# Kernel optimization log

Measured on AMD Instinct MI355X. Metric: run time of the kernel, lower is better.

The kernel has to match this reference:

```python
import jax, jax.numpy as jnp
import numpy as np

NUM_ITEMS = 50000
EMB = 16
SLATE = 10
HID = 512
LAT = 64
RESP = 1024
BATCH = 256


def _linear_params(k, out_dim, in_dim):
    kw, kb = jax.random.split(k)
    s = 1.0 / np.sqrt(in_dim)
    W = jax.random.uniform(kw, (out_dim, in_dim), jnp.float32, -s, s)
    b = jax.random.uniform(kb, (out_dim,), jnp.float32, -s, s)
    return W, b


def setup_inputs() -> dict:
    key = jax.random.key(0)
    ks = jax.random.split(key, 10)
    user_repr = jax.random.randint(ks[0], (BATCH, NUM_ITEMS), 0, 2, dtype=jnp.int32)
    slate = jax.random.randint(ks[1], (BATCH, SLATE), 0, NUM_ITEMS, dtype=jnp.int32)
    response_encoded = jax.random.uniform(ks[2], (BATCH, RESP), jnp.float32)
    eps = jax.random.normal(ks[3], (BATCH, LAT), jnp.float32)
    emb = jax.random.normal(ks[4], (NUM_ITEMS, EMB), jnp.float32)
    in_enc = SLATE * EMB + EMB + RESP
    W_enc, b_enc = _linear_params(ks[5], HID, in_enc)
    W_mu, b_mu = _linear_params(ks[6], LAT, HID)
    W_lv, b_lv = _linear_params(ks[7], LAT, HID)
    in_dec = LAT + EMB + RESP
    W_d1, b_d1 = _linear_params(ks[8], HID, in_dec)
    W_d2, b_d2 = _linear_params(ks[9], SLATE * EMB, HID)
    return {"user_repr": user_repr, "slate": slate, "response_encoded": response_encoded,
            "eps": eps, "emb": emb, "W_enc": W_enc, "b_enc": b_enc,
            "W_mu": W_mu, "b_mu": b_mu, "W_lv": W_lv, "b_lv": b_lv,
            "W_d1": W_d1, "b_d1": b_d1, "W_d2": W_d2, "b_d2": b_d2}


def reference(user_repr, slate, response_encoded, eps, emb,
              W_enc, b_enc, W_mu, b_mu, W_lv, b_lv, W_d1, b_d1, W_d2, b_d2):
    # Ragged embedding-mean pooling over interacted items (vectorized segment mean):
    # mean of emb rows where user_repr==1  ==  (indicator @ emb) / count
    uf = user_repr.astype(jnp.float32)                       # [B, N]
    counts = jnp.sum(uf, axis=1, keepdims=True)              # [B, 1]
    user = (uf @ emb) / counts                               # [B, E]

    cond = jnp.concatenate([user, response_encoded], axis=1)  # [B, E+R]
    slate_emb = emb[slate]                                    # [B, K, E]
    slate_vec = slate_emb.reshape(-1, SLATE * EMB)            # [B, K*E]
    x = jnp.concatenate([slate_vec, cond], axis=1)

    # encoder
    h = jax.nn.relu(x @ W_enc.T + b_enc)
    z_mean = h @ W_mu.T + b_mu
    z_log_var = h @ W_lv.T + b_lv

    # reparameterized sample
    z = z_mean + eps * jnp.exp(0.5 * z_log_var)

    # decoder
    dz = jnp.concatenate([z, cond], axis=1)
    dh = jax.nn.relu(dz @ W_d1.T + b_d1)
    rx = jax.nn.relu(dh @ W_d2.T + b_d2)                      # [B, K*E]
    rx = rx.reshape(-1, SLATE, EMB)                           # [B, K, E]

    # scores vs all items, softmax over items
    logits = jnp.einsum('bkh,nh->bkn', rx, emb)               # [B, K, N]
    probs = jax.nn.softmax(logits, axis=2)
    recon_slate = jnp.argmax(probs, axis=2)                   # [B, K]
    recon_resp = jnp.take_along_axis(probs, slate[:, :, None], axis=2)[..., 0]  # [B, K]
    return z_mean, z_log_var, recon_slate, recon_resp
```

## Files before the change

### kernel.cpp

```cpp
#include <hip/hip_runtime.h>

#define NITEMS 50000
#define EMBD   16
#define NSLATE 10
#define HIDD   512
#define LATD   64
#define RESPD  1024
#define BATCH  256
#define PCHUNK 3125
#define LOG2E  1.44269504088896340736f
#define SHIFT  64.0f

#define NCOL   2560
#define NT     1563
#define IC     64
#define TPC    25

#define OUT_ZM 0
#define OUT_ZLV 16384
#define OUT_RS 32768
#define OUT_RR 35328

#define WS_X    0
#define WS_DZ   307200
#define WS_P2   0
#define WS_PP   589824
#define WS_PART 589824
#define WS_PS   589824
#define WS_PM   753664
#define WS_PA   917504
#define WS_RX   1114112
#define WS_RXS0 1155072
#define WS_RXS1 1175552
#define WS_RXS2 1196032

typedef __attribute__((ext_vector_type(8))) short bfrag;
typedef __attribute__((ext_vector_type(16))) float f32x16;

__device__ __forceinline__ float bfround(float v) {
  unsigned u = __float_as_uint(v);
  unsigned r = (u + 0x7FFFu + ((u >> 16) & 1u)) & 0xFFFF0000u;
  return __uint_as_float(r);
}
__device__ __forceinline__ float bftrunc(float v) {
  return __uint_as_float(__float_as_uint(v) & 0xFFFF0000u);
}
__device__ __forceinline__ short bf16bits(float v) {
  return (short)(__float_as_uint(v) >> 16);
}

__global__ __launch_bounds__(256) void pool_part(const int* __restrict__ u,
    const float* __restrict__ emb, float* __restrict__ pp) {
  int b = blockIdx.x, c = blockIdx.y, t = threadIdx.x;
  float acc[16];
  #pragma unroll
  for (int i = 0; i < 16; ++i) acc[i] = 0.0f;
  float cnt = 0.0f;
  const int* ub = u + (size_t)b * NITEMS;
  int n1 = c * PCHUNK + PCHUNK;
  for (int n = c * PCHUNK + t; n < n1; n += 256) {
    if (ub[n]) {
      const float4* e4 = (const float4*)(emb + (size_t)n * 16);
      float4 a = e4[0], bb = e4[1], cc = e4[2], dd = e4[3];
      acc[0] += a.x;  acc[1] += a.y;  acc[2] += a.z;  acc[3] += a.w;
      acc[4] += bb.x; acc[5] += bb.y; acc[6] += bb.z; acc[7] += bb.w;
      acc[8] += cc.x; acc[9] += cc.y; acc[10] += cc.z; acc[11] += cc.w;
      acc[12] += dd.x; acc[13] += dd.y; acc[14] += dd.z; acc[15] += dd.w;
      cnt += 1.0f;
    }
  }
  #pragma unroll
  for (int off = 32; off > 0; off >>= 1) {
    #pragma unroll
    for (int i = 0; i < 16; ++i) acc[i] += __shfl_down(acc[i], off);
    cnt += __shfl_down(cnt, off);
  }
  int lane = t & 63, wv = t >> 6;
  if (lane == 0) {
    float* dst = pp + ((size_t)(b * 16 + c) * 4 + wv) * 17;
    #pragma unroll
    for (int i = 0; i < 16; ++i) dst[i] = acc[i];
    dst[16] = cnt;
  }
}

__global__ __launch_bounds__(256) void build_x(const float* __restrict__ pp,
    const int* __restrict__ slate, const float* __restrict__ resp,
    const float* __restrict__ emb, float* __restrict__ x, float* __restrict__ dz) {
  __shared__ float fin[17];
  int b = blockIdx.x, t = threadIdx.x;
  if (t < 17) {
    float a = 0.f;
    const float* p = pp + (size_t)b * 64 * 17 + t;
    #pragma unroll
    for (int w = 0; w < 64; ++w) a += p[w * 17];
    fin[t] = a;
  }
  __syncthreads();
  float inv = 1.0f / fin[16];
  if (t < 16) {
    float uv = fin[t] * inv;
    x[b * 1200 + 160 + t] = uv;
    dz[b * 1104 + 64 + t] = uv;
  }
  if (t >= 32 && t < 192) {
    int i = t - 32;
    int k = i >> 4, e = i & 15;
    int it = slate[b * 10 + k];
    x[b * 1200 + i] = emb[(size_t)it * 16 + e];
  }
  for (int i = t; i < 1024; i += 256) {
    float r = resp[b * 1024 + i];
    x[b * 1200 + 176 + i] = r;
    dz[b * 1104 + 80 + i] = r;
  }
}

__global__ __launch_bounds__(256) void gemm64(const float* __restrict__ A,
    const float* __restrict__ B, float* __restrict__ P, int M, int N, int K, int kChunk) {
  __shared__ float As[16][68];
  __shared__ float Bs[16][68];
  int tid = threadIdx.x;
  int m0 = blockIdx.y * 64, n0 = blockIdx.x * 64;
  int ks = blockIdx.z * kChunk;
  int ke = ks + kChunk; if (ke > K) ke = K;
  int sr = tid >> 2;
  int sc = (tid & 3) * 4;
  int tx = tid & 15, ty = tid >> 4;
  float acc[4][4];
  #pragma unroll
  for (int i = 0; i < 4; ++i)
    #pragma unroll
    for (int j = 0; j < 4; ++j) acc[i][j] = 0.f;
  for (int k0 = ks; k0 < ke; k0 += 16) {
    float4 av = make_float4(0.f, 0.f, 0.f, 0.f);
    float4 bv = make_float4(0.f, 0.f, 0.f, 0.f);
    if (k0 + sc < ke)
      av = *(const float4*)(A + (size_t)(m0 + sr) * K + k0 + sc);
    if (k0 + sc < ke && n0 + sr < N)
      bv = *(const float4*)(B + (size_t)(n0 + sr) * K + k0 + sc);
    __syncthreads();
    As[sc][sr] = av.x; As[sc + 1][sr] = av.y; As[sc + 2][sr] = av.z; As[sc + 3][sr] = av.w;
    Bs[sc][sr] = bv.x; Bs[sc + 1][sr] = bv.y; Bs[sc + 2][sr] = bv.z; Bs[sc + 3][sr] = bv.w;
    __syncthreads();
    #pragma unroll
    for (int kk = 0; kk < 16; ++kk) {
      float4 a4 = *(const float4*)&As[kk][4 * ty];
      float4 b4 = *(const float4*)&Bs[kk][4 * tx];
      float a[4] = {a4.x, a4.y, a4.z, a4.w};
      float b[4] = {b4.x, b4.y, b4.z, b4.w};
      #pragma unroll
      for (int i = 0; i < 4; ++i)
        #pragma unroll
        for (int j = 0; j < 4; ++j) acc[i][j] = fmaf(a[i], b[j], acc[i][j]);
    }
  }
  float* Pz = P + (size_t)blockIdx.z * M * N;
  #pragma unroll
  for (int i = 0; i < 4; ++i) {
    int m = m0 + 4 * ty + i, n = n0 + 4 * tx;
    if (n < N)
      *(float4*)(Pz + (size_t)m * N + n) = make_float4(acc[i][0], acc[i][1], acc[i][2], acc[i][3]);
  }
}

__global__ __launch_bounds__(128) void mulv_z_kernel(const float* __restrict__ part,
    const float* __restrict__ benc,
    const float* __restrict__ Wmu, const float* __restrict__ bmu,
    const float* __restrict__ Wlv, const float* __restrict__ blv,
    const float* __restrict__ eps, float* __restrict__ out, float* __restrict__ dz) {
  __shared__ __align__(16) float hs[512];
  __shared__ float zms[64], zlvs[64];
  int b = blockIdx.x, t = threadIdx.x;
  for (int i = t; i < 512; i += 128) {
    float a = benc[i];
    #pragma unroll
    for (int s = 0; s < 4; ++s) a += part[(size_t)s * 131072 + b * 512 + i];
    hs[i] = fmaxf(a, 0.f);
  }
  __syncthreads();
  const float* Wr = (t < 64) ? (Wmu + (size_t)t * 512) : (Wlv + (size_t)(t - 64) * 512);
  float bias = (t < 64) ? bmu[t] : blv[t - 64];
  const float4* w4 = (const float4*)Wr;
  const float4* h4 = (const float4*)hs;
  float a0 = 0.f, a1 = 0.f, a2 = 0.f, a3 = 0.f;
  #pragma unroll 4
  for (int i = 0; i < 128; ++i) {
    float4 w = w4[i], hv = h4[i];
    a0 = fmaf(w.x, hv.x, a0); a1 = fmaf(w.y, hv.y, a1);
    a2 = fmaf(w.z, hv.z, a2); a3 = fmaf(w.w, hv.w, a3);
  }
  float acc = (a0 + a1) + (a2 + a3) + bias;
  if (t < 64) { out[OUT_ZM + b * 64 + t] = acc; zms[t] = acc; }
  else        { out[OUT_ZLV + b * 64 + (t - 64)] = acc; zlvs[t - 64] = acc; }
  __syncthreads();
  if (t < 64) {
    float zv = fmaf(eps[b * 64 + t], __builtin_amdgcn_exp2f(0.7213475204444817f * zlvs[t]), zms[t]);
    dz[b * 1104 + t] = zv;
  }
}

__global__ __launch_bounds__(256) void gemm_d2(const float* __restrict__ part,
    const float* __restrict__ bd1, const float* __restrict__ W, float* __restrict__ p2) {
  __shared__ float As[16][68];
  __shared__ float Bs[16][68];
  const int N = 160;
  int tid = threadIdx.x;
  int m0 = blockIdx.y * 64, n0 = blockIdx.x * 64;
  int ks = blockIdx.z * 64, ke = ks + 64;
  int sr = tid >> 2, sc = (tid & 3) * 4;
  int tx = tid & 15, ty = tid >> 4;
  float acc[4][4];
  #pragma unroll
  for (int i = 0; i < 4; ++i)
    #pragma unroll
    for (int j = 0; j < 4; ++j) acc[i][j] = 0.f;
  for (int k0 = ks; k0 < ke; k0 += 16) {
    int col = k0 + sc;
    const float* p = part + (size_t)(m0 + sr) * 512 + col;
    float4 a0 = *(const float4*)(p);
    float4 a1 = *(const float4*)(p + 131072);
    float4 a2 = *(const float4*)(p + 262144);
    float4 a3 = *(const float4*)(p + 393216);
    float4 bb = *(const float4*)(bd1 + col);
    float4 av;
    av.x = fmaxf(a0.x + a1.x + a2.x + a3.x + bb.x, 0.f);
    av.y = fmaxf(a0.y + a1.y + a2.y + a3.y + bb.y, 0.f);
    av.z = fmaxf(a0.z + a1.z + a2.z + a3.z + bb.z, 0.f);
    av.w = fmaxf(a0.w + a1.w + a2.w + a3.w + bb.w, 0.f);
    float4 bv = make_float4(0.f, 0.f, 0.f, 0.f);
    if (n0 + sr < N)
      bv = *(const float4*)(W + (size_t)(n0 + sr) * 512 + col);
    __syncthreads();
    As[sc][sr] = av.x; As[sc + 1][sr] = av.y; As[sc + 2][sr] = av.z; As[sc + 3][sr] = av.w;
    Bs[sc][sr] = bv.x; Bs[sc + 1][sr] = bv.y; Bs[sc + 2][sr] = bv.z; Bs[sc + 3][sr] = bv.w;
    __syncthreads();
    #pragma unroll
    for (int kk = 0; kk < 16; ++kk) {
      float4 a4 = *(const float4*)&As[kk][4 * ty];
      float4 b4 = *(const float4*)&Bs[kk][4 * tx];
      float a[4] = {a4.x, a4.y, a4.z, a4.w};
      float b[4] = {b4.x, b4.y, b4.z, b4.w};
      #pragma unroll
      for (int i = 0; i < 4; ++i)
        #pragma unroll
        for (int j = 0; j < 4; ++j) acc[i][j] = fmaf(a[i], b[j], acc[i][j]);
    }
  }
  float* Pz = p2 + (size_t)blockIdx.z * 40960;
  #pragma unroll
  for (int i = 0; i < 4; ++i) {
    int m = m0 + 4 * ty + i, n = n0 + 4 * tx;
    if (n < N)
      *(float4*)(Pz + (size_t)m * 160 + n) = make_float4(acc[i][0], acc[i][1], acc[i][2], acc[i][3]);
  }
}

__global__ __launch_bounds__(256) void rx_prep(const float* __restrict__ p2,
    const float* __restrict__ bd2, float* __restrict__ rx,
    unsigned short* __restrict__ rx0, unsigned short* __restrict__ rx1,
    unsigned short* __restrict__ rx2) {
  int b = blockIdx.x, t = threadIdx.x;
  if (t >= 160) return;
  float a = bd2[t];
  #pragma unroll
  for (int z = 0; z < 8; ++z) a += p2[(size_t)z * 40960 + b * 160 + t];
  float v = fmaxf(a, 0.f) * LOG2E;
  rx[b * 160 + t] = v;
  int col = b * 10 + (t >> 4), e = t & 15;
  float f0 = bfround(v);
  float d1 = v - f0;
  float f1 = bfround(d1);
  float d2 = d1 - f1;
  float f2 = bfround(d2);
  rx0[col * 16 + e] = (unsigned short)(__float_as_uint(f0) >> 16);
  rx1[col * 16 + e] = (unsigned short)(__float_as_uint(f1) >> 16);
  rx2[col * 16 + e] = (unsigned short)(__float_as_uint(f2) >> 16);
}

__global__ __launch_bounds__(256) void score_mfma(const float* __restrict__ emb,
    const unsigned short* __restrict__ rx0, const unsigned short* __restrict__ rx1,
    const unsigned short* __restrict__ rx2,
    float* __restrict__ ps, float* __restrict__ pm, int* __restrict__ pa) {
  int t = threadIdx.x;
  int w = t >> 6, l = t & 63;
  int ln = l & 31, hf = l >> 5;
  int cg = blockIdx.x * 4 + w;
  int ic = blockIdx.y;
  int col = cg * 32 + ln;
  size_t boff = (size_t)col * 16 + hf * 8;
  bfrag b0 = *(const bfrag*)(rx0 + boff);
  bfrag b1 = *(const bfrag*)(rx1 + boff);
  bfrag b2 = *(const bfrag*)(rx2 + boff);
  float s_acc = 0.f, mmax = -3.402823466e38f;
  int am = 0x7FFFFFFF;
  int ts = ic * TPC, te = ts + TPC;
  if (te > NT) te = NT;
  #pragma unroll 1
  for (int tile = ts; tile < te; ++tile) {
    int r = tile * 32 + ln;
    float4 e0, e1;
    if (r < NITEMS) {
      const float4* p = (const float4*)(emb + (size_t)r * 16 + hf * 8);
      e0 = p[0]; e1 = p[1];
    } else {
      e0 = make_float4(-128.f, -128.f, -128.f, -128.f);
      e1 = e0;
    }
    float ev[8] = {e0.x, e0.y, e0.z, e0.w, e1.x, e1.y, e1.z, e1.w};
    bfrag a0, a1, a2;
    #pragma unroll
    for (int i = 0; i < 8; ++i) {
      float v = ev[i];
      float f0 = bfround(v);
      float d1 = v - f0;
      float f1 = bftrunc(d1);
      float d2 = d1 - f1;
      a0[i] = bf16bits(f0);
      a1[i] = bf16bits(f1);
      a2[i] = bf16bits(d2);
    }
    f32x16 acc;
    #pragma unroll
    for (int i = 0; i < 16; ++i) acc[i] = -SHIFT;
    acc = __builtin_amdgcn_mfma_f32_32x32x16_bf16(a1, b1, acc, 0, 0, 0);
    acc = __builtin_amdgcn_mfma_f32_32x32x16_bf16(a2, b0, acc, 0, 0, 0);
    acc = __builtin_amdgcn_mfma_f32_32x32x16_bf16(a0, b2, acc, 0, 0, 0);
    acc = __builtin_amdgcn_mfma_f32_32x32x16_bf16(a1, b0, acc, 0, 0, 0);
    acc = __builtin_amdgcn_mfma_f32_32x32x16_bf16(a0, b1, acc, 0, 0, 0);
    acc = __builtin_amdgcn_mfma_f32_32x32x16_bf16(a0, b0, acc, 0, 0, 0);
    int base = tile * 32 + 4 * hf;
    #pragma unroll
    for (int g = 0; g < 4; ++g) {
      #pragma unroll
      for (int q = 0; q < 4; ++q) {
        float x = acc[g * 4 + q];
        s_acc += __builtin_amdgcn_exp2f(x);
        if (x > mmax) { mmax = x; am = base + 8 * g + q; }
      }
    }
  }
  s_acc += __shfl_xor(s_acc, 32);
  float om = __shfl_xor(mmax, 32);
  int oa = __shfl_xor(am, 32);
  if (om > mmax || (om == mmax && oa < am)) { mmax = om; am = oa; }
  if (hf == 0) {
    int idx = ic * NCOL + col;
    ps[idx] = s_acc; pm[idx] = mmax; pa[idx] = am;
  }
}

__global__ __launch_bounds__(256) void score_final(const float* __restrict__ psg,
    const float* __restrict__ pmg, const int* __restrict__ pag,
    const float* __restrict__ rx, const float* __restrict__ emb,
    const int* __restrict__ slate, float* __restrict__ out) {
  int tid = blockIdx.x * 256 + threadIdx.x;
  if (tid >= BATCH * 10) return;
  int b = tid / 10, k = tid % 10;
  float S = 0.f, M = -3.402823466e38f;
  int AM = 2147483647;
  for (int c = 0; c < IC; ++c) {
    int idx = c * NCOL + tid;
    S += psg[idx];
    float m2 = pmg[idx];
    int oa = pag[idx];
    bool take = (m2 > M) || (m2 == M && oa < AM);
    AM = take ? oa : AM;
    M = fmaxf(M, m2);
  }
  int it = slate[b * 10 + k];
  const float* er = emb + (size_t)it * 16;
  const float* rr = rx + b * 160 + k * 16;
  float xs = -SHIFT;
  #pragma unroll
  for (int e = 0; e < 16; ++e) xs = fmaf(rr[e], er[e], xs);
  out[OUT_RS + b * 10 + k] = (float)AM;
  out[OUT_RR + b * 10 + k] = __builtin_amdgcn_exp2f(xs) / S;
}

extern "C" void kernel_launch(void* const* d_in, const int* in_sizes, int n_in,
                              void* d_out, int out_size, void* d_ws, size_t ws_size,
                              hipStream_t stream) {
  const int* user_repr = (const int*)d_in[0];
  const int* slate = (const int*)d_in[1];
  const float* resp = (const float*)d_in[2];
  const float* eps = (const float*)d_in[3];
  const float* emb = (const float*)d_in[4];
  const float* W_enc = (const float*)d_in[5];
  const float* b_enc = (const float*)d_in[6];
  const float* W_mu = (const float*)d_in[7];
  const float* b_mu = (const float*)d_in[8];
  const float* W_lv = (const float*)d_in[9];
  const float* b_lv = (const float*)d_in[10];
  const float* W_d1 = (const float*)d_in[11];
  const float* b_d1 = (const float*)d_in[12];
  const float* W_d2 = (const float*)d_in[13];
  const float* b_d2 = (const float*)d_in[14];
  float* out = (float*)d_out;
  float* ws = (float*)d_ws;

  float* x    = ws + WS_X;
  float* dz   = ws + WS_DZ;
  float* p2   = ws + WS_P2;
  float* pp   = ws + WS_PP;
  float* part = ws + WS_PART;
  float* ps   = ws + WS_PS;
  float* pmb  = ws + WS_PM;
  int*   pab  = (int*)(ws + WS_PA);
  float* rx   = ws + WS_RX;
  unsigned short* rx0 = (unsigned short*)(ws + WS_RXS0);
  unsigned short* rx1 = (unsigned short*)(ws + WS_RXS1);
  unsigned short* rx2 = (unsigned short*)(ws + WS_RXS2);

  pool_part<<<dim3(256, 16), 256, 0, stream>>>(user_repr, emb, pp);
  build_x<<<256, 256, 0, stream>>>(pp, slate, resp, emb, x, dz);
  gemm64<<<dim3(8, 4, 4), 256, 0, stream>>>(x, W_enc, part, 256, 512, 1200, 300);
  mulv_z_kernel<<<256, 128, 0, stream>>>(part, b_enc, W_mu, b_mu, W_lv, b_lv, eps, out, dz);
  gemm64<<<dim3(8, 4, 4), 256, 0, stream>>>(dz, W_d1, part, 256, 512, 1104, 276);
  gemm_d2<<<dim3(3, 4, 8), 256, 0, stream>>>(part, b_d1, W_d2, p2);
  rx_prep<<<256, 256, 0, stream>>>(p2, b_d2, rx, rx0, rx1, rx2);
  score_mfma<<<dim3(20, IC), 256, 0, stream>>>(emb, rx0, rx1, rx2, ps, pmb, pab);
  score_final<<<10, 256, 0, stream>>>(ps, pmb, pab, rx, emb, slate, out);
}
```

Before: 286.7 us.

## Compute two column tiles per wave in score kernel, cheaper bf16 split, finer item chunks

Each wave now handles 64 output columns (two 32-wide MFMA tiles), so the emb rows it loads and splits into three bf16 parts are reused across both tiles, halving per-column load and conversion work. The bf16 split now truncates instead of rounding for the top part and packs pairs with bit operations, which cuts ALU instructions. The item-chunk count is doubled (IC 128, TPC 13) to keep enough blocks in flight, and the partial-result workspace is relocated to fit the larger buffers. Trade-offs are higher register pressure from two accumulators, and a final reduction over twice as many partials.

After: 281.5 us. No clear change (-1.8%).

```diff
diff --git a/kernel.cpp b/kernel.cpp
--- a/kernel.cpp
+++ b/kernel.cpp
@@ -13,8 +13,8 @@
 
 #define NCOL   2560
 #define NT     1563
-#define IC     64
-#define TPC    25
+#define IC     128
+#define TPC    13
 
 #define OUT_ZM 0
 #define OUT_ZLV 16384
@@ -24,11 +24,11 @@
 #define WS_X    0
 #define WS_DZ   307200
 #define WS_P2   0
+#define WS_PS   0
+#define WS_PM   327680
+#define WS_PA   655360
 #define WS_PP   589824
 #define WS_PART 589824
-#define WS_PS   589824
-#define WS_PM   753664
-#define WS_PA   917504
 #define WS_RX   1114112
 #define WS_RXS0 1155072
 #define WS_RXS1 1175552
@@ -41,12 +41,6 @@
   unsigned u = __float_as_uint(v);
   unsigned r = (u + 0x7FFFu + ((u >> 16) & 1u)) & 0xFFFF0000u;
   return __uint_as_float(r);
-}
-__device__ __forceinline__ float bftrunc(float v) {
-  return __uint_as_float(__float_as_uint(v) & 0xFFFF0000u);
-}
-__device__ __forceinline__ short bf16bits(float v) {
-  return (short)(__float_as_uint(v) >> 16);
 }
 
 __global__ __launch_bounds__(256) void pool_part(const int* __restrict__ u,
@@ -285,15 +279,21 @@
   int t = threadIdx.x;
   int w = t >> 6, l = t & 63;
   int ln = l & 31, hf = l >> 5;
-  int cg = blockIdx.x * 4 + w;
+  int pair = blockIdx.x * 4 + w;
   int ic = blockIdx.y;
-  int col = cg * 32 + ln;
-  size_t boff = (size_t)col * 16 + hf * 8;
-  bfrag b0 = *(const bfrag*)(rx0 + boff);
-  bfrag b1 = *(const bfrag*)(rx1 + boff);
-  bfrag b2 = *(const bfrag*)(rx2 + boff);
-  float s_acc = 0.f, mmax = -3.402823466e38f;
-  int am = 0x7FFFFFFF;
+  int colA = pair * 64 + ln;
+  int colB = colA + 32;
+  size_t offA = (size_t)colA * 16 + hf * 8;
+  size_t offB = (size_t)colB * 16 + hf * 8;
+  bfrag bA0 = *(const bfrag*)(rx0 + offA);
+  bfrag bA1 = *(const bfrag*)(rx1 + offA);
+  bfrag bA2 = *(const bfrag*)(rx2 + offA);
+  bfrag bB0 = *(const bfrag*)(rx0 + offB);
+  bfrag bB1 = *(const bfrag*)(rx1 + offB);
+  bfrag bB2 = *(const bfrag*)(rx2 + offB);
+  float sA = 0.f, sB = 0.f;
+  float mA = -3.402823466e38f, mB = -3.402823466e38f;
+  int aA = 0x7FFFFFFF, aB = 0x7FFFFFFF;
   int ts = ic * TPC, te = ts + TPC;
   if (te > NT) te = NT;
   #pragma unroll 1
@@ -308,45 +308,61 @@
       e1 = e0;
     }
     float ev[8] = {e0.x, e0.y, e0.z, e0.w, e1.x, e1.y, e1.z, e1.w};
-    bfrag a0, a1, a2;
-    #pragma unroll
-    for (int i = 0; i < 8; ++i) {
-      float v = ev[i];
-      float f0 = bfround(v);
-      float d1 = v - f0;
-      float f1 = bftrunc(d1);
-      float d2 = d1 - f1;
-      a0[i] = bf16bits(f0);
-      a1[i] = bf16bits(f1);
-      a2[i] = bf16bits(d2);
-    }
-    f32x16 acc;
-    #pragma unroll
-    for (int i = 0; i < 16; ++i) acc[i] = -SHIFT;
-    acc = __builtin_amdgcn_mfma_f32_32x32x16_bf16(a1, b1, acc, 0, 0, 0);
-    acc = __builtin_amdgcn_mfma_f32_32x32x16_bf16(a2, b0, acc, 0, 0, 0);
-    acc = __builtin_amdgcn_mfma_f32_32x32x16_bf16(a0, b2, acc, 0, 0, 0);
-    acc = __builtin_amdgcn_mfma_f32_32x32x16_bf16(a1, b0, acc, 0, 0, 0);
-    acc = __builtin_amdgcn_mfma_f32_32x32x16_bf16(a0, b1, acc, 0, 0, 0);
-    acc = __builtin_amdgcn_mfma_f32_32x32x16_bf16(a0, b0, acc, 0, 0, 0);
+    union { bfrag f; unsigned u[4]; } A0, A1, A2;
+    #pragma unroll
+    for (int j = 0; j < 4; ++j) {
+      float v0 = ev[2 * j], v1 = ev[2 * j + 1];
+      unsigned u0 = __float_as_uint(v0), u1 = __float_as_uint(v1);
+      A0.u[j] = (u0 >> 16) | (u1 & 0xFFFF0000u);
+      float r0 = v0 - __uint_as_float(u0 & 0xFFFF0000u);
+      float r1 = v1 - __uint_as_float(u1 & 0xFFFF0000u);
+      unsigned w0 = __float_as_uint(r0), w1 = __float_as_uint(r1);
+      A1.u[j] = (w0 >> 16) | (w1 & 0xFFFF0000u);
+      float q0 = r0 - __uint_as_float(w0 & 0xFFFF0000u);
+      float q1 = r1 - __uint_as_float(w1 & 0xFFFF0000u);
+      A2.u[j] = (__float_as_uint(q0) >> 16) | (__float_as_uint(q1) & 0xFFFF0000u);
+    }
+    f32x16 accA, accB;
+    #pragma unroll
+    for (int i = 0; i < 16; ++i) { accA[i] = -SHIFT; accB[i] = -SHIFT; }
+    accA = __builtin_amdgcn_mfma_f32_32x32x16_bf16(A1.f, bA1, accA, 0, 0, 0);
+    accB = __builtin_amdgcn_mfma_f32_32x32x16_bf16(A1.f, bB1, accB, 0, 0, 0);
+    accA = __builtin_amdgcn_mfma_f32_32x32x16_bf16(A2.f, bA0, accA, 0, 0, 0);
+    accB = __builtin_amdgcn_mfma_f32_32x32x16_bf16(A2.f, bB0, accB, 0, 0, 0);
+    accA = __builtin_amdgcn_mfma_f32_32x32x16_bf16(A0.f, bA2, accA, 0, 0, 0);
+    accB = __builtin_amdgcn_mfma_f32_32x32x16_bf16(A0.f, bB2, accB, 0, 0, 0);
+    accA = __builtin_amdgcn_mfma_f32_32x32x16_bf16(A1.f, bA0, accA, 0, 0, 0);
+    accB = __builtin_amdgcn_mfma_f32_32x32x16_bf16(A1.f, bB0, accB, 0, 0, 0);
+    accA = __builtin_amdgcn_mfma_f32_32x32x16_bf16(A0.f, bA1, accA, 0, 0, 0);
+    accB = __builtin_amdgcn_mfma_f32_32x32x16_bf16(A0.f, bB1, accB, 0, 0, 0);
+    accA = __builtin_amdgcn_mfma_f32_32x32x16_bf16(A0.f, bA0, accA, 0, 0, 0);
+    accB = __builtin_amdgcn_mfma_f32_32x32x16_bf16(A0.f, bB0, accB, 0, 0, 0);
     int base = tile * 32 + 4 * hf;
     #pragma unroll
     for (int g = 0; g < 4; ++g) {
       #pragma unroll
       for (int q = 0; q < 4; ++q) {
-        float x = acc[g * 4 + q];
-        s_acc += __builtin_amdgcn_exp2f(x);
-        if (x > mmax) { mmax = x; am = base + 8 * g + q; }
+        int idx = base + 8 * g + q;
+        float xa = accA[g * 4 + q];
+        sA += __builtin_amdgcn_exp2f(xa);
+        if (xa > mA) { mA = xa; aA = idx; }
+        float xb = accB[g * 4 + q];
+        sB += __builtin_amdgcn_exp2f(xb);
+        if (xb > mB) { mB = xb; aB = idx; }
       }
     }
   }
-  s_acc += __shfl_xor(s_acc, 32);
-  float om = __shfl_xor(mmax, 32);
-  int oa = __shfl_xor(am, 32);
-  if (om > mmax || (om == mmax && oa < am)) { mmax = om; am = oa; }
+  sA += __shfl_xor(sA, 32);
+  sB += __shfl_xor(sB, 32);
+  float omA = __shfl_xor(mA, 32); int oaA = __shfl_xor(aA, 32);
+  if (omA > mA || (omA == mA && oaA < aA)) { mA = omA; aA = oaA; }
+  float omB = __shfl_xor(mB, 32); int oaB = __shfl_xor(aB, 32);
+  if (omB > mB || (omB == mB && oaB < aB)) { mB = omB; aB = oaB; }
   if (hf == 0) {
-    int idx = ic * NCOL + col;
-    ps[idx] = s_acc; pm[idx] = mmax; pa[idx] = am;
+    int idxA = ic * NCOL + colA;
+    int idxB = ic * NCOL + colB;
+    ps[idxA] = sA; pm[idxA] = mA; pa[idxA] = aA;
+    ps[idxB] = sB; pm[idxB] = mB; pa[idxB] = aB;
   }
 }
 
@@ -419,6 +435,6 @@
   gemm64<<<dim3(8, 4, 4), 256, 0, stream>>>(dz, W_d1, part, 256, 512, 1104, 276);
   gemm_d2<<<dim3(3, 4, 8), 256, 0, stream>>>(part, b_d1, W_d2, p2);
   rx_prep<<<256, 256, 0, stream>>>(p2, b_d2, rx, rx0, rx1, rx2);
-  score_mfma<<<dim3(20, IC), 256, 0, stream>>>(emb, rx0, rx1, rx2, ps, pmb, pab);
+  score_mfma<<<dim3(10, IC), 256, 0, stream>>>(emb, rx0, rx1, rx2, ps, pmb, pab);
   score_final<<<10, 256, 0, stream>>>(ps, pmb, pab, rx, emb, slate, out);
 }
```
